# Kernel tuning notes

Hardware: AMD Instinct MI355X
Metric: run time of the kernel (lower is better)

The kernel has to match this reference:

```python
import jax, jax.numpy as jnp
import numpy as np

NUM_HEAD = 8
A_DIM = 256
M_DIM = 256
OUT_DIM = 256
KEY_DIM = A_DIM // NUM_HEAD   # 32
VALUE_DIM = M_DIM // NUM_HEAD # 32
B, NQ, NK = 128, 384, 384


def setup_inputs() -> dict:
    key = jax.random.key(0)
    ks = jax.random.split(key, 11)
    s = 0.05
    return {
        "q_data": jax.random.normal(ks[0], (B, NQ, A_DIM), jnp.float32),
        "m_data": jax.random.normal(ks[1], (B, NK, M_DIM), jnp.float32),
        "bias": jax.random.normal(ks[2], (B, NQ, NK), jnp.float32),
        "nonbatched_bias": jax.random.normal(ks[3], (NQ, NK), jnp.float32),
        "query_w": jax.random.normal(ks[4], (A_DIM, NUM_HEAD, KEY_DIM), jnp.float32) * s,
        "key_w": jax.random.normal(ks[5], (M_DIM, NUM_HEAD, KEY_DIM), jnp.float32) * s,
        "value_w": jax.random.normal(ks[6], (M_DIM, NUM_HEAD, VALUE_DIM), jnp.float32) * s,
        "gating_w": jax.random.normal(ks[7], (A_DIM, NUM_HEAD, VALUE_DIM), jnp.float32) * s,
        "gating_b": jax.random.normal(ks[8], (NUM_HEAD, VALUE_DIM), jnp.float32) * s,
        "output_w": jax.random.normal(ks[9], (NUM_HEAD, VALUE_DIM, OUT_DIM), jnp.float32) * s,
        "output_b": jax.random.normal(ks[10], (OUT_DIM,), jnp.float32) * s,
    }


def reference(q_data, m_data, bias, nonbatched_bias, query_w, key_w, value_w,
              gating_w, gating_b, output_w, output_b):
    # q: [b, q, h, c] scaled by 1/sqrt(key_dim)
    scale = KEY_DIM ** -0.5
    q = jnp.einsum('bqa,ahc->bqhc', q_data, query_w) * scale
    k = jnp.einsum('bka,ahc->bkhc', m_data, key_w)
    v = jnp.einsum('bka,ahc->bkhc', m_data, value_w)
    # logits [b, h, q, k] with per-batch bias and shared nonbatched bias
    logits = jnp.einsum('bqhc,bkhc->bhqk', q, k)
    logits = logits + bias[:, None, :, :] + nonbatched_bias[None, None, :, :]
    weights = jax.nn.softmax(logits, axis=-1)
    weighted_avg = jnp.einsum('bhqk,bkhc->bqhc', weights, v)
    # sigmoid gating
    gate = jax.nn.sigmoid(jnp.einsum('bqa,ahc->bqhc', q_data, gating_w)
                          + gating_b[None, None, :, :])
    weighted_avg = weighted_avg * gate
    # output projection
    out = jnp.einsum('bqhc,hco->bqo', weighted_avg, output_w) + output_b
    return out
```

## Files before the change

kernel.cpp:

```cpp
#include <hip/hip_runtime.h>

typedef unsigned short u16;
typedef unsigned int u32;
typedef __attribute__((ext_vector_type(8))) short bf16x8;
typedef __attribute__((ext_vector_type(4))) float f32x4;

#define BATCH 128
#define NQL   384
#define NKL   384
#define NHEAD 8
#define HD    32
#define ADIM  256

__device__ __forceinline__ u16 f2bf(float f) {
    union { float f; u32 u; } v; v.f = f;
    u32 r = v.u + 0x7fffu + ((v.u >> 16) & 1u);
    return (u16)(r >> 16);
}
__device__ __forceinline__ float bf2f(u16 u) {
    union { u32 u; float f; } v; v.u = ((u32)u) << 16;
    return v.f;
}
__device__ __forceinline__ u32 pk(float a, float b) {
    return (u32)f2bf(a) | ((u32)f2bf(b) << 16);
}

__global__ __launch_bounds__(256) void prep_w_kernel(
    const float* __restrict__ qw, const float* __restrict__ kw,
    const float* __restrict__ vw, const float* __restrict__ gw,
    const float* __restrict__ ow, u16* __restrict__ wt)
{
    const float* src;
    switch (blockIdx.y) {
        case 0: src = qw; break;
        case 1: src = kw; break;
        case 2: src = vw; break;
        case 3: src = gw; break;
        default: src = ow; break;
    }
    u16* dst = wt + (size_t)blockIdx.y * 65536;
    int t = threadIdx.x;
    int n0 = blockIdx.x * 16;
    for (int i = 0; i < 16; i++) {
        int n = n0 + i;
        dst[n * 256 + t] = f2bf(src[t * 256 + n]);
    }
}

__global__ __launch_bounds__(256) void proj4_kernel(
    const float* __restrict__ qd, const float* __restrict__ md,
    const u16* __restrict__ wt, const float* __restrict__ gb,
    u16* __restrict__ q_o, u16* __restrict__ k_o,
    u16* __restrict__ v_o, u16* __restrict__ g_o)
{
    const int z = blockIdx.z;
    const float* A = (z == 0 || z == 3) ? qd : md;
    const u16* W = wt + (size_t)z * 65536;
    u16* O = (z == 0) ? q_o : (z == 1) ? k_o : (z == 2) ? v_o : g_o;

    const int bm = blockIdx.x * 128, bn = blockIdx.y * 128;
    const int tid = threadIdx.x;
    const int lane = tid & 63, wave = tid >> 6;
    const int col = lane & 15, quad = lane >> 4;
    const int mw = (wave & 1) * 64, nw = (wave >> 1) * 64;

    __shared__ u16 As[128][32];
    __shared__ u16 Ws[128][32];

    f32x4 acc[4][4];
#pragma unroll
    for (int i = 0; i < 4; i++)
#pragma unroll
        for (int j = 0; j < 4; j++) acc[i][j] = (f32x4){0.f, 0.f, 0.f, 0.f};

    const int arow = tid >> 1, acb = (tid & 1) * 16;
    const float* asrc = A + (size_t)(bm + arow) * 256 + acb;
    const u16*   wsrc = W + (size_t)(bn + arow) * 256 + acb;

    for (int k0 = 0; k0 < 256; k0 += 32) {
        __syncthreads();
        {
            float4 f0 = *(const float4*)(asrc + k0 + 0);
            float4 f1 = *(const float4*)(asrc + k0 + 4);
            float4 f2 = *(const float4*)(asrc + k0 + 8);
            float4 f3 = *(const float4*)(asrc + k0 + 12);
            uint4 u0 = make_uint4(pk(f0.x, f0.y), pk(f0.z, f0.w), pk(f1.x, f1.y), pk(f1.z, f1.w));
            uint4 u1 = make_uint4(pk(f2.x, f2.y), pk(f2.z, f2.w), pk(f3.x, f3.y), pk(f3.z, f3.w));
            *(uint4*)&As[arow][acb + 0] = u0;
            *(uint4*)&As[arow][acb + 8] = u1;
            *(uint4*)&Ws[arow][acb + 0] = *(const uint4*)(wsrc + k0 + 0);
            *(uint4*)&Ws[arow][acb + 8] = *(const uint4*)(wsrc + k0 + 8);
        }
        __syncthreads();
        bf16x8 bv[4];
#pragma unroll
        for (int nt = 0; nt < 4; nt++)
            bv[nt] = *(const bf16x8*)&Ws[nw + nt * 16 + col][quad * 8];
#pragma unroll
        for (int mt = 0; mt < 4; mt++) {
            bf16x8 av = *(const bf16x8*)&As[mw + mt * 16 + col][quad * 8];
#pragma unroll
            for (int nt = 0; nt < 4; nt++)
                acc[mt][nt] = __builtin_amdgcn_mfma_f32_16x16x32_bf16(av, bv[nt], acc[mt][nt], 0, 0, 0);
        }
    }

#pragma unroll
    for (int nt = 0; nt < 4; nt++) {
        int gn = bn + nw + nt * 16 + col;
        float gbv = (z == 3) ? gb[gn] : 0.f;
#pragma unroll
        for (int mt = 0; mt < 4; mt++) {
#pragma unroll
            for (int r = 0; r < 4; r++) {
                int gm = bm + mw + mt * 16 + quad * 4 + r;
                float v = acc[mt][nt][r];
                if (z == 0) v *= 0.17677669529663689f;
                if (z == 3) v = 1.f / (1.f + __expf(-(v + gbv)));
                O[(size_t)gm * 256 + gn] = f2bf(v);
            }
        }
    }
}

__global__ __launch_bounds__(256) void attn_kernel(
    const u16* __restrict__ q_ws, const u16* __restrict__ k_ws,
    const u16* __restrict__ v_ws, const u16* __restrict__ g_ws,
    const float* __restrict__ bias, const float* __restrict__ nb,
    u16* __restrict__ wa_ws)
{
    const int b = blockIdx.z, h = blockIdx.y;
    const int tid = threadIdx.x;
    const int lane = tid & 63, wave = tid >> 6;
    const int col = lane & 15, quad = lane >> 4;
    const int q0 = blockIdx.x * 64 + wave * 16;

    __shared__ u16 Ks[384][32];
    __shared__ u16 Vt[32][392];
    __shared__ u16 Ps[4][16][72];

    const u16* kg = k_ws + ((size_t)b * 384) * 256 + h * 32;
    const u16* vg = v_ws + ((size_t)b * 384) * 256 + h * 32;
    for (int f = tid * 8; f < 384 * 32; f += 256 * 8) {
        int kr = f >> 5, c = f & 31;
        *(uint4*)&Ks[kr][c] = *(const uint4*)&kg[kr * 256 + c];
    }
    for (int f = tid * 8; f < 384 * 32; f += 256 * 8) {
        int kv = f >> 5, c = f & 31;
        u16 tmp[8];
        *(uint4*)tmp = *(const uint4*)&vg[kv * 256 + c];
#pragma unroll
        for (int j = 0; j < 8; j++) Vt[c + j][kv] = tmp[j];
    }
    __syncthreads();

    const u16* qg = q_ws + ((size_t)(b * 384 + q0 + col)) * 256 + h * 32 + quad * 8;
    bf16x8 qf = *(const bf16x8*)qg;

    float S[24][4];
#pragma unroll
    for (int t = 0; t < 24; t++) {
        bf16x8 kf = *(const bf16x8*)&Ks[t * 16 + col][quad * 8];
        f32x4 a = (f32x4){0.f, 0.f, 0.f, 0.f};
        a = __builtin_amdgcn_mfma_f32_16x16x32_bf16(qf, kf, a, 0, 0, 0);
        S[t][0] = a[0]; S[t][1] = a[1]; S[t][2] = a[2]; S[t][3] = a[3];
    }

    const float* bp  = bias + ((size_t)b * 384 + q0 + quad * 4) * 384 + col;
    const float* nbp = nb + (size_t)(q0 + quad * 4) * 384 + col;
#pragma unroll
    for (int r = 0; r < 4; r++) {
#pragma unroll
        for (int t = 0; t < 24; t++)
            S[t][r] += bp[r * 384 + t * 16] + nbp[r * 384 + t * 16];
    }

#pragma unroll
    for (int r = 0; r < 4; r++) {
        float m = S[0][r];
#pragma unroll
        for (int t = 1; t < 24; t++) m = fmaxf(m, S[t][r]);
#pragma unroll
        for (int o = 1; o < 16; o <<= 1) m = fmaxf(m, __shfl_xor(m, o));
        float s = 0.f;
#pragma unroll
        for (int t = 0; t < 24; t++) { float p = __expf(S[t][r] - m); S[t][r] = p; s += p; }
#pragma unroll
        for (int o = 1; o < 16; o <<= 1) s += __shfl_xor(s, o);
        float inv = 1.f / s;
#pragma unroll
        for (int t = 0; t < 24; t++) S[t][r] *= inv;
    }

    f32x4 o0 = (f32x4){0.f, 0.f, 0.f, 0.f};
    f32x4 o1 = (f32x4){0.f, 0.f, 0.f, 0.f};
    for (int g = 0; g < 6; g++) {
#pragma unroll
        for (int tt = 0; tt < 4; tt++) {
            int t = g * 4 + tt;
#pragma unroll
            for (int r = 0; r < 4; r++)
                Ps[wave][quad * 4 + r][tt * 16 + col] = f2bf(S[t][r]);
        }
        asm volatile("s_waitcnt lgkmcnt(0)" ::: "memory");
        bf16x8 a0 = *(const bf16x8*)&Ps[wave][col][quad * 8];
        bf16x8 a1 = *(const bf16x8*)&Ps[wave][col][32 + quad * 8];
        bf16x8 b00 = *(const bf16x8*)&Vt[col][g * 64 + quad * 8];
        bf16x8 b01 = *(const bf16x8*)&Vt[col][g * 64 + 32 + quad * 8];
        bf16x8 b10 = *(const bf16x8*)&Vt[16 + col][g * 64 + quad * 8];
        bf16x8 b11 = *(const bf16x8*)&Vt[16 + col][g * 64 + 32 + quad * 8];
        o0 = __builtin_amdgcn_mfma_f32_16x16x32_bf16(a0, b00, o0, 0, 0, 0);
        o0 = __builtin_amdgcn_mfma_f32_16x16x32_bf16(a1, b01, o0, 0, 0, 0);
        o1 = __builtin_amdgcn_mfma_f32_16x16x32_bf16(a0, b10, o1, 0, 0, 0);
        o1 = __builtin_amdgcn_mfma_f32_16x16x32_bf16(a1, b11, o1, 0, 0, 0);
        asm volatile("s_waitcnt lgkmcnt(0)" ::: "memory");
    }

    const size_t rowbase = (size_t)b * 384 + q0 + quad * 4;
#pragma unroll
    for (int r = 0; r < 4; r++) {
        size_t base = (rowbase + r) * 256 + h * 32;
        {
            size_t idx = base + col;
            wa_ws[idx] = f2bf(o0[r] * bf2f(g_ws[idx]));
        }
        {
            size_t idx = base + 16 + col;
            wa_ws[idx] = f2bf(o1[r] * bf2f(g_ws[idx]));
        }
    }
}

__global__ __launch_bounds__(256) void outproj_kernel(
    const u16* __restrict__ wa, const u16* __restrict__ W,
    const float* __restrict__ ob, float* __restrict__ out)
{
    const int bm = blockIdx.x * 128, bn = blockIdx.y * 128;
    const int tid = threadIdx.x;
    const int lane = tid & 63, wave = tid >> 6;
    const int col = lane & 15, quad = lane >> 4;
    const int mw = (wave & 1) * 64, nw = (wave >> 1) * 64;

    __shared__ u16 As[128][32];
    __shared__ u16 Ws[128][32];

    f32x4 acc[4][4];
#pragma unroll
    for (int i = 0; i < 4; i++)
#pragma unroll
        for (int j = 0; j < 4; j++) acc[i][j] = (f32x4){0.f, 0.f, 0.f, 0.f};

    const int arow = tid >> 1, acb = (tid & 1) * 16;
    const u16* asrc = wa + (size_t)(bm + arow) * 256 + acb;
    const u16* wsrc = W + (size_t)(bn + arow) * 256 + acb;

    for (int k0 = 0; k0 < 256; k0 += 32) {
        __syncthreads();
        *(uint4*)&As[arow][acb + 0] = *(const uint4*)(asrc + k0 + 0);
        *(uint4*)&As[arow][acb + 8] = *(const uint4*)(asrc + k0 + 8);
        *(uint4*)&Ws[arow][acb + 0] = *(const uint4*)(wsrc + k0 + 0);
        *(uint4*)&Ws[arow][acb + 8] = *(const uint4*)(wsrc + k0 + 8);
        __syncthreads();
        bf16x8 bv[4];
#pragma unroll
        for (int nt = 0; nt < 4; nt++)
            bv[nt] = *(const bf16x8*)&Ws[nw + nt * 16 + col][quad * 8];
#pragma unroll
        for (int mt = 0; mt < 4; mt++) {
            bf16x8 av = *(const bf16x8*)&As[mw + mt * 16 + col][quad * 8];
#pragma unroll
            for (int nt = 0; nt < 4; nt++)
                acc[mt][nt] = __builtin_amdgcn_mfma_f32_16x16x32_bf16(av, bv[nt], acc[mt][nt], 0, 0, 0);
        }
    }

#pragma unroll
    for (int nt = 0; nt < 4; nt++) {
        int gn = bn + nw + nt * 16 + col;
        float obv = ob[gn];
#pragma unroll
        for (int mt = 0; mt < 4; mt++) {
#pragma unroll
            for (int r = 0; r < 4; r++) {
                int gm = bm + mw + mt * 16 + quad * 4 + r;
                out[(size_t)gm * 256 + gn] = acc[mt][nt][r] + obv;
            }
        }
    }
}

extern "C" void kernel_launch(void* const* d_in, const int* in_sizes, int n_in,
                              void* d_out, int out_size, void* d_ws, size_t ws_size,
                              hipStream_t stream)
{
    const float* q_data = (const float*)d_in[0];
    const float* m_data = (const float*)d_in[1];
    const float* bias   = (const float*)d_in[2];
    const float* nb     = (const float*)d_in[3];
    const float* qw     = (const float*)d_in[4];
    const float* kw     = (const float*)d_in[5];
    const float* vw     = (const float*)d_in[6];
    const float* gw     = (const float*)d_in[7];
    const float* gb     = (const float*)d_in[8];
    const float* ow     = (const float*)d_in[9];
    const float* ob     = (const float*)d_in[10];
    float* out = (float*)d_out;

    char* ws = (char*)d_ws;
    u16* wt = (u16*)ws;
    const size_t PROJ = (size_t)BATCH * NQL * 256;
    u16* q_ws  = (u16*)(ws + (1 << 20));
    u16* k_ws  = q_ws + PROJ;
    u16* v_ws  = k_ws + PROJ;
    u16* g_ws  = v_ws + PROJ;
    u16* wa_ws = g_ws + PROJ;

    prep_w_kernel<<<dim3(16, 5), 256, 0, stream>>>(qw, kw, vw, gw, ow, wt);
    proj4_kernel<<<dim3(384, 2, 4), 256, 0, stream>>>(q_data, m_data, wt, gb,
                                                      q_ws, k_ws, v_ws, g_ws);
    attn_kernel<<<dim3(6, 8, 128), 256, 0, stream>>>(q_ws, k_ws, v_ws, g_ws,
                                                     bias, nb, wa_ws);
    outproj_kernel<<<dim3(384, 2), 256, 0, stream>>>(wa_ws, wt + 4 * 65536, ob, out);
}
```

Before: 464.9 us.

## Share activation tiles across paired projections and load K/V once per head in attention

```diff
diff --git a/kernel.cpp b/kernel.cpp
--- a/kernel.cpp
+++ b/kernel.cpp
@@ -11,6 +11,7 @@
 #define NHEAD 8
 #define HD    32
 #define ADIM  256
+#define QSCALE 0.17677669529663689f
 
 __device__ __forceinline__ u16 f2bf(float f) {
     union { float f; u32 u; } v; v.f = f;
@@ -47,16 +48,18 @@
     }
 }
 
-__global__ __launch_bounds__(256) void proj4_kernel(
+__global__ __launch_bounds__(256) void proj2_kernel(
     const float* __restrict__ qd, const float* __restrict__ md,
     const u16* __restrict__ wt, const float* __restrict__ gb,
     u16* __restrict__ q_o, u16* __restrict__ k_o,
     u16* __restrict__ v_o, u16* __restrict__ g_o)
 {
     const int z = blockIdx.z;
-    const float* A = (z == 0 || z == 3) ? qd : md;
-    const u16* W = wt + (size_t)z * 65536;
-    u16* O = (z == 0) ? q_o : (z == 1) ? k_o : (z == 2) ? v_o : g_o;
+    const float* A = (z == 0) ? qd : md;
+    const u16* W0 = wt + (size_t)(z == 0 ? 0 : 1) * 65536;
+    const u16* W1 = wt + (size_t)(z == 0 ? 3 : 2) * 65536;
+    u16* O0 = (z == 0) ? q_o : k_o;
+    u16* O1 = (z == 0) ? g_o : v_o;
 
     const int bm = blockIdx.x * 128, bn = blockIdx.y * 128;
     const int tid = threadIdx.x;
@@ -65,17 +68,22 @@
     const int mw = (wave & 1) * 64, nw = (wave >> 1) * 64;
 
     __shared__ u16 As[128][32];
-    __shared__ u16 Ws[128][32];
-
-    f32x4 acc[4][4];
+    __shared__ u16 Ws0[128][32];
+    __shared__ u16 Ws1[128][32];
+
+    f32x4 acc0[4][4], acc1[4][4];
 #pragma unroll
     for (int i = 0; i < 4; i++)
 #pragma unroll
-        for (int j = 0; j < 4; j++) acc[i][j] = (f32x4){0.f, 0.f, 0.f, 0.f};
+        for (int j = 0; j < 4; j++) {
+            acc0[i][j] = (f32x4){0.f, 0.f, 0.f, 0.f};
+            acc1[i][j] = (f32x4){0.f, 0.f, 0.f, 0.f};
+        }
 
     const int arow = tid >> 1, acb = (tid & 1) * 16;
     const float* asrc = A + (size_t)(bm + arow) * 256 + acb;
-    const u16*   wsrc = W + (size_t)(bn + arow) * 256 + acb;
+    const u16*   ws0  = W0 + (size_t)(bn + arow) * 256 + acb;
+    const u16*   ws1  = W1 + (size_t)(bn + arow) * 256 + acb;
 
     for (int k0 = 0; k0 < 256; k0 += 32) {
         __syncthreads();
@@ -88,36 +96,46 @@
             uint4 u1 = make_uint4(pk(f2.x, f2.y), pk(f2.z, f2.w), pk(f3.x, f3.y), pk(f3.z, f3.w));
             *(uint4*)&As[arow][acb + 0] = u0;
             *(uint4*)&As[arow][acb + 8] = u1;
-            *(uint4*)&Ws[arow][acb + 0] = *(const uint4*)(wsrc + k0 + 0);
-            *(uint4*)&Ws[arow][acb + 8] = *(const uint4*)(wsrc + k0 + 8);
+            *(uint4*)&Ws0[arow][acb + 0] = *(const uint4*)(ws0 + k0 + 0);
+            *(uint4*)&Ws0[arow][acb + 8] = *(const uint4*)(ws0 + k0 + 8);
+            *(uint4*)&Ws1[arow][acb + 0] = *(const uint4*)(ws1 + k0 + 0);
+            *(uint4*)&Ws1[arow][acb + 8] = *(const uint4*)(ws1 + k0 + 8);
         }
         __syncthreads();
-        bf16x8 bv[4];
-#pragma unroll
-        for (int nt = 0; nt < 4; nt++)
-            bv[nt] = *(const bf16x8*)&Ws[nw + nt * 16 + col][quad * 8];
+        bf16x8 bv0[4], bv1[4];
+#pragma unroll
+        for (int nt = 0; nt < 4; nt++) {
+            bv0[nt] = *(const bf16x8*)&Ws0[nw + nt * 16 + col][quad * 8];
+            bv1[nt] = *(const bf16x8*)&Ws1[nw + nt * 16 + col][quad * 8];
+        }
 #pragma unroll
         for (int mt = 0; mt < 4; mt++) {
             bf16x8 av = *(const bf16x8*)&As[mw + mt * 16 + col][quad * 8];
 #pragma unroll
-            for (int nt = 0; nt < 4; nt++)
-                acc[mt][nt] = __builtin_amdgcn_mfma_f32_16x16x32_bf16(av, bv[nt], acc[mt][nt], 0, 0, 0);
+            for (int nt = 0; nt < 4; nt++) {
+                acc0[mt][nt] = __builtin_amdgcn_mfma_f32_16x16x32_bf16(av, bv0[nt], acc0[mt][nt], 0, 0, 0);
+                acc1[mt][nt] = __builtin_amdgcn_mfma_f32_16x16x32_bf16(av, bv1[nt], acc1[mt][nt], 0, 0, 0);
+            }
         }
     }
 
 #pragma unroll
     for (int nt = 0; nt < 4; nt++) {
         int gn = bn + nw + nt * 16 + col;
-        float gbv = (z == 3) ? gb[gn] : 0.f;
+        float gbv = (z == 0) ? gb[gn] : 0.f;
 #pragma unroll
         for (int mt = 0; mt < 4; mt++) {
 #pragma unroll
             for (int r = 0; r < 4; r++) {
                 int gm = bm + mw + mt * 16 + quad * 4 + r;
-                float v = acc[mt][nt][r];
-                if (z == 0) v *= 0.17677669529663689f;
-                if (z == 3) v = 1.f / (1.f + __expf(-(v + gbv)));
-                O[(size_t)gm * 256 + gn] = f2bf(v);
+                float v0 = acc0[mt][nt][r];
+                float v1 = acc1[mt][nt][r];
+                if (z == 0) {
+                    v0 *= QSCALE;
+                    v1 = 1.f / (1.f + __expf(-(v1 + gbv)));
+                }
+                O0[(size_t)gm * 256 + gn] = f2bf(v0);
+                O1[(size_t)gm * 256 + gn] = f2bf(v1);
             }
         }
     }
@@ -129,104 +147,127 @@
     const float* __restrict__ bias, const float* __restrict__ nb,
     u16* __restrict__ wa_ws)
 {
-    const int b = blockIdx.z, h = blockIdx.y;
+    const int bi = blockIdx.x >> 3, h = blockIdx.x & 7;
     const int tid = threadIdx.x;
     const int lane = tid & 63, wave = tid >> 6;
     const int col = lane & 15, quad = lane >> 4;
-    const int q0 = blockIdx.x * 64 + wave * 16;
 
     __shared__ u16 Ks[384][32];
-    __shared__ u16 Vt[32][392];
-    __shared__ u16 Ps[4][16][72];
-
-    const u16* kg = k_ws + ((size_t)b * 384) * 256 + h * 32;
-    const u16* vg = v_ws + ((size_t)b * 384) * 256 + h * 32;
+    __shared__ u16 Vt[32 * 384];
+    __shared__ __align__(16) char scratch[4][4096];
+    float* Bs = (float*)scratch[wave];
+    u16*   Ps = (u16*)scratch[wave];
+
+    const u16* kg = k_ws + (size_t)bi * 384 * 256 + h * 32;
+    const u16* vg = v_ws + (size_t)bi * 384 * 256 + h * 32;
     for (int f = tid * 8; f < 384 * 32; f += 256 * 8) {
         int kr = f >> 5, c = f & 31;
         *(uint4*)&Ks[kr][c] = *(const uint4*)&kg[kr * 256 + c];
     }
     for (int f = tid * 8; f < 384 * 32; f += 256 * 8) {
-        int kv = f >> 5, c = f & 31;
+        int kv = f >> 5, c0 = f & 31;
         u16 tmp[8];
-        *(uint4*)tmp = *(const uint4*)&vg[kv * 256 + c];
-#pragma unroll
-        for (int j = 0; j < 8; j++) Vt[c + j][kv] = tmp[j];
+        *(uint4*)tmp = *(const uint4*)&vg[kv * 256 + c0];
+        int kvg = kv >> 3, kvr = kv & 7;
+#pragma unroll
+        for (int j = 0; j < 8; j++) {
+            int c = c0 + j;
+            Vt[c * 384 + ((kvg ^ (c & 7)) << 3) + kvr] = tmp[j];
+        }
     }
     __syncthreads();
 
-    const u16* qg = q_ws + ((size_t)(b * 384 + q0 + col)) * 256 + h * 32 + quad * 8;
-    bf16x8 qf = *(const bf16x8*)qg;
-
-    float S[24][4];
-#pragma unroll
-    for (int t = 0; t < 24; t++) {
-        bf16x8 kf = *(const bf16x8*)&Ks[t * 16 + col][quad * 8];
-        f32x4 a = (f32x4){0.f, 0.f, 0.f, 0.f};
-        a = __builtin_amdgcn_mfma_f32_16x16x32_bf16(qf, kf, a, 0, 0, 0);
-        S[t][0] = a[0]; S[t][1] = a[1]; S[t][2] = a[2]; S[t][3] = a[3];
-    }
-
-    const float* bp  = bias + ((size_t)b * 384 + q0 + quad * 4) * 384 + col;
-    const float* nbp = nb + (size_t)(q0 + quad * 4) * 384 + col;
-#pragma unroll
-    for (int r = 0; r < 4; r++) {
-#pragma unroll
-        for (int t = 0; t < 24; t++)
-            S[t][r] += bp[r * 384 + t * 16] + nbp[r * 384 + t * 16];
-    }
-
-#pragma unroll
-    for (int r = 0; r < 4; r++) {
-        float m = S[0][r];
-#pragma unroll
-        for (int t = 1; t < 24; t++) m = fmaxf(m, S[t][r]);
-#pragma unroll
-        for (int o = 1; o < 16; o <<= 1) m = fmaxf(m, __shfl_xor(m, o));
-        float s = 0.f;
-#pragma unroll
-        for (int t = 0; t < 24; t++) { float p = __expf(S[t][r] - m); S[t][r] = p; s += p; }
-#pragma unroll
-        for (int o = 1; o < 16; o <<= 1) s += __shfl_xor(s, o);
-        float inv = 1.f / s;
-#pragma unroll
-        for (int t = 0; t < 24; t++) S[t][r] *= inv;
-    }
-
-    f32x4 o0 = (f32x4){0.f, 0.f, 0.f, 0.f};
-    f32x4 o1 = (f32x4){0.f, 0.f, 0.f, 0.f};
-    for (int g = 0; g < 6; g++) {
-#pragma unroll
-        for (int tt = 0; tt < 4; tt++) {
-            int t = g * 4 + tt;
-#pragma unroll
-            for (int r = 0; r < 4; r++)
-                Ps[wave][quad * 4 + r][tt * 16 + col] = f2bf(S[t][r]);
-        }
-        asm volatile("s_waitcnt lgkmcnt(0)" ::: "memory");
-        bf16x8 a0 = *(const bf16x8*)&Ps[wave][col][quad * 8];
-        bf16x8 a1 = *(const bf16x8*)&Ps[wave][col][32 + quad * 8];
-        bf16x8 b00 = *(const bf16x8*)&Vt[col][g * 64 + quad * 8];
-        bf16x8 b01 = *(const bf16x8*)&Vt[col][g * 64 + 32 + quad * 8];
-        bf16x8 b10 = *(const bf16x8*)&Vt[16 + col][g * 64 + quad * 8];
-        bf16x8 b11 = *(const bf16x8*)&Vt[16 + col][g * 64 + 32 + quad * 8];
-        o0 = __builtin_amdgcn_mfma_f32_16x16x32_bf16(a0, b00, o0, 0, 0, 0);
-        o0 = __builtin_amdgcn_mfma_f32_16x16x32_bf16(a1, b01, o0, 0, 0, 0);
-        o1 = __builtin_amdgcn_mfma_f32_16x16x32_bf16(a0, b10, o1, 0, 0, 0);
-        o1 = __builtin_amdgcn_mfma_f32_16x16x32_bf16(a1, b11, o1, 0, 0, 0);
-        asm volatile("s_waitcnt lgkmcnt(0)" ::: "memory");
-    }
-
-    const size_t rowbase = (size_t)b * 384 + q0 + quad * 4;
-#pragma unroll
-    for (int r = 0; r < 4; r++) {
-        size_t base = (rowbase + r) * 256 + h * 32;
-        {
-            size_t idx = base + col;
-            wa_ws[idx] = f2bf(o0[r] * bf2f(g_ws[idx]));
-        }
-        {
-            size_t idx = base + 16 + col;
-            wa_ws[idx] = f2bf(o1[r] * bf2f(g_ws[idx]));
+    for (int qt = wave; qt < 24; qt += 4) {
+        const int q0 = qt * 16;
+        bf16x8 qf = *(const bf16x8*)(q_ws + ((size_t)(bi * 384 + q0 + col)) * 256 + h * 32 + quad * 8);
+
+        const float* brow = bias + ((size_t)bi * 384 + q0) * 384;
+        const float* nrow = nb + (size_t)q0 * 384;
+
+        float S[24][4];
+#pragma unroll
+        for (int g = 0; g < 6; g++) {
+#pragma unroll
+            for (int i = 0; i < 4; i++) {
+                int flat = lane + 64 * i;
+                int row = flat >> 4, c4 = (flat & 15) << 2;
+                float4 bv = *(const float4*)&brow[(size_t)row * 384 + g * 64 + c4];
+                float4 nv = *(const float4*)&nrow[(size_t)row * 384 + g * 64 + c4];
+                float4 sv = make_float4(bv.x + nv.x, bv.y + nv.y, bv.z + nv.z, bv.w + nv.w);
+                *(float4*)&Bs[row * 64 + c4] = sv;
+            }
+            asm volatile("s_waitcnt lgkmcnt(0)" ::: "memory");
+#pragma unroll
+            for (int tt = 0; tt < 4; tt++) {
+                int t = g * 4 + tt;
+                f32x4 ci;
+#pragma unroll
+                for (int r = 0; r < 4; r++)
+                    ci[r] = Bs[(quad * 4 + r) * 64 + tt * 16 + col];
+                bf16x8 kf = *(const bf16x8*)&Ks[t * 16 + col][quad * 8];
+                f32x4 a = __builtin_amdgcn_mfma_f32_16x16x32_bf16(qf, kf, ci, 0, 0, 0);
+                S[t][0] = a[0]; S[t][1] = a[1]; S[t][2] = a[2]; S[t][3] = a[3];
+            }
+            asm volatile("s_waitcnt lgkmcnt(0)" ::: "memory");
+        }
+
+#pragma unroll
+        for (int r = 0; r < 4; r++) {
+            float m = S[0][r];
+#pragma unroll
+            for (int t = 1; t < 24; t++) m = fmaxf(m, S[t][r]);
+#pragma unroll
+            for (int o = 1; o < 16; o <<= 1) m = fmaxf(m, __shfl_xor(m, o));
+            float s = 0.f;
+#pragma unroll
+            for (int t = 0; t < 24; t++) { float p = __expf(S[t][r] - m); S[t][r] = p; s += p; }
+#pragma unroll
+            for (int o = 1; o < 16; o <<= 1) s += __shfl_xor(s, o);
+            float inv = 1.f / s;
+#pragma unroll
+            for (int t = 0; t < 24; t++) S[t][r] *= inv;
+        }
+
+        f32x4 o0 = (f32x4){0.f, 0.f, 0.f, 0.f};
+        f32x4 o1 = (f32x4){0.f, 0.f, 0.f, 0.f};
+#pragma unroll
+        for (int g = 0; g < 6; g++) {
+#pragma unroll
+            for (int tt = 0; tt < 4; tt++) {
+                int t = g * 4 + tt;
+#pragma unroll
+                for (int r = 0; r < 4; r++)
+                    Ps[(quad * 4 + r) * 72 + tt * 16 + col] = f2bf(S[t][r]);
+            }
+            asm volatile("s_waitcnt lgkmcnt(0)" ::: "memory");
+            bf16x8 a0 = *(const bf16x8*)&Ps[col * 72 + quad * 8];
+            bf16x8 a1 = *(const bf16x8*)&Ps[col * 72 + 32 + quad * 8];
+            const int e = col & 7;
+            const int gg0 = g * 8 + quad;
+            const int gg1 = gg0 + 4;
+            bf16x8 b00 = *(const bf16x8*)&Vt[col * 384 + ((gg0 ^ e) << 3)];
+            bf16x8 b01 = *(const bf16x8*)&Vt[col * 384 + ((gg1 ^ e) << 3)];
+            bf16x8 b10 = *(const bf16x8*)&Vt[(col + 16) * 384 + ((gg0 ^ e) << 3)];
+            bf16x8 b11 = *(const bf16x8*)&Vt[(col + 16) * 384 + ((gg1 ^ e) << 3)];
+            o0 = __builtin_amdgcn_mfma_f32_16x16x32_bf16(a0, b00, o0, 0, 0, 0);
+            o0 = __builtin_amdgcn_mfma_f32_16x16x32_bf16(a1, b01, o0, 0, 0, 0);
+            o1 = __builtin_amdgcn_mfma_f32_16x16x32_bf16(a0, b10, o1, 0, 0, 0);
+            o1 = __builtin_amdgcn_mfma_f32_16x16x32_bf16(a1, b11, o1, 0, 0, 0);
+            asm volatile("s_waitcnt lgkmcnt(0)" ::: "memory");
+        }
+
+        const size_t rowbase = (size_t)bi * 384 + q0 + quad * 4;
+#pragma unroll
+        for (int r = 0; r < 4; r++) {
+            size_t base = (rowbase + r) * 256 + h * 32;
+            {
+                size_t idx = base + col;
+                wa_ws[idx] = f2bf(o0[r] * bf2f(g_ws[idx]));
+            }
+            {
+                size_t idx = base + 16 + col;
+                wa_ws[idx] = f2bf(o1[r] * bf2f(g_ws[idx]));
+            }
         }
     }
 }
@@ -316,9 +357,9 @@
     u16* wa_ws = g_ws + PROJ;
 
     prep_w_kernel<<<dim3(16, 5), 256, 0, stream>>>(qw, kw, vw, gw, ow, wt);
-    proj4_kernel<<<dim3(384, 2, 4), 256, 0, stream>>>(q_data, m_data, wt, gb,
+    proj2_kernel<<<dim3(384, 2, 2), 256, 0, stream>>>(q_data, m_data, wt, gb,
                                                       q_ws, k_ws, v_ws, g_ws);
-    attn_kernel<<<dim3(6, 8, 128), 256, 0, stream>>>(q_ws, k_ws, v_ws, g_ws,
-                                                     bias, nb, wa_ws);
+    attn_kernel<<<dim3(1024), 256, 0, stream>>>(q_ws, k_ws, v_ws, g_ws,
+                                                bias, nb, wa_ws);
     outproj_kernel<<<dim3(384, 2), 256, 0, stream>>>(wa_ws, wt + 4 * 65536, ob, out);
 }
```

New measurement: 445.5 us. -4.2%, faster.
